# Kernel tuning notes

Hardware: AMD Instinct MI355X
Metric: run time of the kernel (lower is better)

## Reference

```python
import jax, jax.numpy as jnp
import numpy as np

N_HEADS = 8

def gcn_conv(x, edge_index, W, b):
    # PyG GCNConv: add self-loops, symmetric normalization, linear transform + bias
    N = x.shape[0]
    loop = jnp.arange(N)
    src = jnp.concatenate([edge_index[0], loop])
    dst = jnp.concatenate([edge_index[1], loop])
    deg = jax.ops.segment_sum(jnp.ones(src.shape[0], dtype=x.dtype), dst, num_segments=N)
    dinv = jax.lax.rsqrt(jnp.maximum(deg, 1.0))  # deg >= 1 due to self-loops
    norm = dinv[src] * dinv[dst]                 # [E+N]
    h = x @ W                                    # [N, out]
    msg = h[src] * norm[:, None]                 # gather + scale
    return jax.ops.segment_sum(msg, dst, num_segments=N) + b

def layer_norm(x, g, b):
    mu = jnp.mean(x, axis=-1, keepdims=True)
    var = jnp.mean((x - mu) ** 2, axis=-1, keepdims=True)
    return (x - mu) * jax.lax.rsqrt(var + 1e-5) * g + b

def mha(q, kv, Wq, Wk, Wv, Wo):
    B, M, d = q.shape
    dh = d // N_HEADS
    Q = (q @ Wq).reshape(B, M, N_HEADS, dh)
    K = (kv @ Wk).reshape(B, kv.shape[1], N_HEADS, dh)
    V = (kv @ Wv).reshape(B, kv.shape[1], N_HEADS, dh)
    scale = jnp.asarray(1.0 / np.sqrt(dh), q.dtype)
    scores = jnp.einsum('bqhd,bkhd->bhqk', Q, K) * scale
    attn = jax.nn.softmax(scores, axis=-1)
    out = jnp.einsum('bhqk,bkhd->bqhd', attn, V).reshape(B, M, d)
    return out @ Wo

def setup_inputs() -> dict:
    key = jax.random.key(0)
    ks = jax.random.split(key, 24)
    B, M, d, dff, L = 32, 1024, 128, 512, 2
    N, E = B * M, 524288
    s = 0.02
    inp = {
        'enc_out_vari': jax.random.normal(ks[0], (B, M, d), jnp.float32),
        'x_enc': jax.random.normal(ks[1], (B, M, d), jnp.float32),
        'x_raw': jax.random.normal(ks[2], (N, d), jnp.float32),
        'edge_index': jax.random.randint(ks[3], (2, E), 0, N, jnp.int64 if jax.config.jax_enable_x64 else jnp.int32),
        'W_gcn1': s * jax.random.normal(ks[4], (d, d), jnp.float32),
        'b_gcn1': jnp.zeros((d,), jnp.float32),
        'W_gcn2': s * jax.random.normal(ks[5], (d, d), jnp.float32),
        'b_gcn2': jnp.zeros((d,), jnp.float32),
        'Wq': s * jax.random.normal(ks[6], (L, d, d), jnp.float32),
        'Wk': s * jax.random.normal(ks[7], (L, d, d), jnp.float32),
        'Wv': s * jax.random.normal(ks[8], (L, d, d), jnp.float32),
        'Wo': s * jax.random.normal(ks[9], (L, d, d), jnp.float32),
        'Wff1': s * jax.random.normal(ks[10], (L, d, dff), jnp.float32),
        'bff1': jnp.zeros((L, dff), jnp.float32),
        'Wff2': s * jax.random.normal(ks[11], (L, dff, d), jnp.float32),
        'bff2': jnp.zeros((L, d), jnp.float32),
        'ln1_g': jnp.ones((L, d), jnp.float32),
        'ln1_b': jnp.zeros((L, d), jnp.float32),
        'ln2_g': jnp.ones((L, d), jnp.float32),
        'ln2_b': jnp.zeros((L, d), jnp.float32),
    }
    return inp

def reference(enc_out_vari, x_enc, x_raw, edge_index, W_gcn1, b_gcn1, W_gcn2, b_gcn2,
              Wq, Wk, Wv, Wo, Wff1, bff1, Wff2, bff2, ln1_g, ln1_b, ln2_g, ln2_b):
    B, M, d = enc_out_vari.shape
    # GCN stack (dropout is identity in eval mode)
    x1 = jax.nn.relu(gcn_conv(x_raw, edge_index, W_gcn1, b_gcn1))
    x2 = jax.nn.relu(gcn_conv(x1, edge_index, W_gcn2, b_gcn2))
    x = x2.reshape(B, M, d)
    # Transformer encoder: cross-attention from enc_out_vari onto GCN features
    y = enc_out_vari
    L = Wq.shape[0]
    for l in range(L):
        a = mha(y, x, Wq[l], Wk[l], Wv[l], Wo[l])
        y = layer_norm(y + a, ln1_g[l], ln1_b[l])
        f = jax.nn.relu(y @ Wff1[l] + bff1[l]) @ Wff2[l] + bff2[l]
        y = layer_norm(y + f, ln2_g[l], ln2_b[l])
    return y
```

## Files before the change

kernel.cpp:

```cpp
#include <hip/hip_runtime.h>
#include <math.h>


typedef __attribute__((ext_vector_type(8)))  short short8;
typedef __attribute__((ext_vector_type(4)))  float f32x4;
typedef __attribute__((ext_vector_type(16))) float f32x16;

__device__ __forceinline__ unsigned short f2bf(float x) {
    unsigned u = __builtin_bit_cast(unsigned, x);
    u = (u + 0x7FFFu + ((u >> 16) & 1u)) >> 16;
    return (unsigned short)u;
}
__device__ __forceinline__ float bflo(unsigned u) { return __builtin_bit_cast(float, u << 16); }
__device__ __forceinline__ float bfhi(unsigned u) { return __builtin_bit_cast(float, u & 0xffff0000u); }
__device__ __forceinline__ float fast_exp2(float x) {
    float r; asm("v_exp_f32 %0, %1" : "=v"(r) : "v"(x)); return r;
}

__global__ void count_kernel(const int* __restrict__ dst, int* __restrict__ cnt, int E) {
    int e = blockIdx.x * 256 + threadIdx.x;
    if (e < E) atomicAdd(&cnt[dst[e]], 1);
}

__global__ __launch_bounds__(256)
void scanA_kernel(const int* __restrict__ cnt, int* __restrict__ partial)
{
    __shared__ int wsum[4];
    int t = threadIdx.x;
    int v = cnt[blockIdx.x * 256 + t];
    #pragma unroll
    for (int off = 32; off; off >>= 1) v += __shfl_xor(v, off, 64);
    if ((t & 63) == 0) wsum[t >> 6] = v;
    __syncthreads();
    if (t == 0) partial[blockIdx.x] = wsum[0] + wsum[1] + wsum[2] + wsum[3];
}

__global__ __launch_bounds__(128)
void scanB_kernel(const int* __restrict__ partial, int* __restrict__ base)
{
    __shared__ int p[128];
    int t = threadIdx.x;
    int v = partial[t];
    p[t] = v;
    __syncthreads();
    for (int o = 1; o < 128; o <<= 1) {
        int q = (t >= o) ? p[t - o] : 0;
        __syncthreads();
        p[t] += q;
        __syncthreads();
    }
    base[t] = p[t] - v;
}

__global__ __launch_bounds__(256)
void scanC_kernel(const int* __restrict__ cnt, const int* __restrict__ base,
                  int* __restrict__ off, int* __restrict__ cursor,
                  float* __restrict__ dinv, int N, int E)
{
    __shared__ int p[256];
    int t = threadIdx.x, b = blockIdx.x;
    int i = b * 256 + t;
    int c = cnt[i];
    p[t] = c;
    __syncthreads();
    for (int o = 1; o < 256; o <<= 1) {
        int q = (t >= o) ? p[t - o] : 0;
        __syncthreads();
        p[t] += q;
        __syncthreads();
    }
    int ex = base[b] + p[t] - c;
    off[i] = ex;
    cursor[i] = ex;
    dinv[i] = rsqrtf((float)c + 1.0f);
    if (b == 0 && t == 0) off[N] = E;
}

__global__ void place_kernel(const int* __restrict__ src, const int* __restrict__ dst,
                             int* __restrict__ cursor, int* __restrict__ csr_src, int E)
{
    int e = blockIdx.x * 256 + threadIdx.x;
    if (e < E) {
        int p = atomicAdd(&cursor[dst[e]], 1);
        csr_src[p] = src[e];
    }
}

__global__ __launch_bounds__(256)
void prep_kernel(const float* __restrict__ xraw, unsigned short* __restrict__ xrawh,
                 const float* __restrict__ enc, float* __restrict__ bufY,
                 unsigned short* __restrict__ bufYh,
                 const float* Wg1, const float* Wg2, const float* Wq, const float* Wk,
                 const float* Wv, const float* Wo, const float* Wff1, const float* Wff2,
                 unsigned short* __restrict__ out, int nconv)
{
    const int bid = blockIdx.x, tid = threadIdx.x;
    if (bid < nconv) {
        int i = bid * 256 + tid;
        float4 v = ((const float4*)xraw)[i];
        ushort4 h; h.x = f2bf(v.x); h.y = f2bf(v.y); h.z = f2bf(v.z); h.w = f2bf(v.w);
        ((ushort4*)xrawh)[i] = h;
        return;
    }
    if (bid < 2 * nconv) {
        int i = (bid - nconv) * 256 + tid;
        float4 v = ((const float4*)enc)[i];
        ((float4*)bufY)[i] = v;
        ushort4 h; h.x = f2bf(v.x); h.y = f2bf(v.y); h.z = f2bf(v.z); h.w = f2bf(v.w);
        ((ushort4*)bufYh)[i] = h;
        return;
    }
    const int bid2 = bid - 2 * nconv;
    const int slot = bid2 >> 8;
    const int bx   = bid2 & 255;
    const float* src; int ks; int Ns; size_t doff; float scale = 1.0f;
    if      (slot == 0)  { src = Wg1;                        ks = 7; Ns = 128; doff = 0; }
    else if (slot == 1)  { src = Wg2;                        ks = 7; Ns = 128; doff = 16384; }
    else if (slot <= 3)  { src = Wq  + (slot - 2)  * 16384;  ks = 7; Ns = 128; doff = 32768  + (size_t)(slot - 2)  * 16384; scale = 0.36067376022f; }
    else if (slot <= 5)  { src = Wk  + (slot - 4)  * 16384;  ks = 7; Ns = 128; doff = 65536  + (size_t)(slot - 4)  * 32768; }
    else if (slot <= 7)  { src = Wv  + (slot - 6)  * 16384;  ks = 7; Ns = 128; doff = 65536  + (size_t)(slot - 6)  * 32768 + 16384; }
    else if (slot <= 9)  { src = Wo  + (slot - 8)  * 16384;  ks = 7; Ns = 128; doff = 131072 + (size_t)(slot - 8)  * 16384; }
    else if (slot <= 11) { src = Wff1 + (slot - 10) * 65536; ks = 7; Ns = 512; doff = 163840 + (size_t)(slot - 10) * 65536; }
    else                 { src = Wff2 + (slot - 12) * 65536; ks = 9; Ns = 128; doff = 294912 + (size_t)(slot - 12) * 65536; }
    const int total = Ns << ks;
    int id = bx * 256 + tid;
    if (id >= total) return;
    int n = id >> ks;
    int k = id & ((1 << ks) - 1);
    out[doff + id] = f2bf(src[(size_t)k * Ns + n] * scale);
}

__device__ __forceinline__
void gemm64_body(unsigned short* As, unsigned short* Ws,
                 const unsigned short* __restrict__ A,
                 const unsigned short* __restrict__ Wt,
                 void* __restrict__ C, void* __restrict__ C2, int K, int ldc,
                 const float* __restrict__ bias, const float* __restrict__ rowscale,
                 int relu, int mode, int bx, int by)
{
    const int tid  = threadIdx.x;
    const int lane = tid & 63, wave = tid >> 6;
    const int m31 = lane & 31, hi = lane >> 5;
    const int row0 = bx * 64;
    const int c0   = by * 64;
    const int wrow = (wave & 1) * 32;
    const int wcol = (wave >> 1) * 32;
    const int sr = tid >> 2, sk = (tid & 3) * 16;

    f32x16 acc = {};

    for (int kt = 0; kt < K; kt += 64) {
        if (kt) __syncthreads();
        *(short8*)&As[sr * 72 + sk]     = *(const short8*)&A [(size_t)(row0 + sr) * K + kt + sk];
        *(short8*)&As[sr * 72 + sk + 8] = *(const short8*)&A [(size_t)(row0 + sr) * K + kt + sk + 8];
        *(short8*)&Ws[sr * 72 + sk]     = *(const short8*)&Wt[(size_t)(c0   + sr) * K + kt + sk];
        *(short8*)&Ws[sr * 72 + sk + 8] = *(const short8*)&Wt[(size_t)(c0   + sr) * K + kt + sk + 8];
        __syncthreads();
        #pragma unroll
        for (int ks = 0; ks < 4; ++ks) {
            short8 af = *(const short8*)&As[(wrow + m31) * 72 + ks * 16 + hi * 8];
            short8 bf = *(const short8*)&Ws[(wcol + m31) * 72 + ks * 16 + hi * 8];
            acc = __builtin_amdgcn_mfma_f32_32x32x16_bf16(af, bf, acc, 0, 0, 0);
        }
    }

    const int col = c0 + wcol + m31;
    #pragma unroll
    for (int r = 0; r < 16; ++r) {
        const int row = row0 + wrow + (r & 3) + 8 * (r >> 2) + 4 * hi;
        float v = acc[r];
        if (rowscale) v *= rowscale[row];
        if (bias) v += bias[col];
        if (relu) v = fmaxf(v, 0.0f);
        if (mode == 1) {
            ((unsigned short*)C)[(size_t)row * ldc + col] = f2bf(v);
        } else {
            if (col < 128) {
                ((unsigned short*)C)[(size_t)row * 128 + col] = f2bf(v);
            } else {
                int ch = col - 128, hh = ch >> 4, dd = ch & 15;
                int kg = row & 1023;
                int w  = kg & 127;
                int kpos = (kg & ~127) | ((w & 15) * 8) | (w >> 4);
                ((unsigned short*)C2)[(((size_t)(row >> 10) * 8 + hh) * 16 + dd) * 1024
                                      + kpos] = f2bf(v);
            }
        }
    }
}

__global__ __launch_bounds__(256)
void gemm64_kernel(const unsigned short* __restrict__ A,
                   const unsigned short* __restrict__ Wt,
                   void* __restrict__ C, void* __restrict__ C2, int K,
                   const float* __restrict__ bias, const float* __restrict__ rowscale,
                   int relu, int mode)
{
    __shared__ unsigned short As[64 * 72];
    __shared__ unsigned short Ws[64 * 72];
    gemm64_body(As, Ws, A, Wt, C, C2, K, gridDim.y * 64, bias, rowscale, relu, mode,
                blockIdx.x, blockIdx.y);
}

__global__ __launch_bounds__(256)
void qkv_kernel(const unsigned short* __restrict__ Yh, const unsigned short* __restrict__ wtq,
                unsigned short* __restrict__ Qh,
                const unsigned short* __restrict__ Bh, const unsigned short* __restrict__ wtkv,
                unsigned short* __restrict__ Kg, unsigned short* __restrict__ Vtg)
{
    __shared__ unsigned short As[64 * 72];
    __shared__ unsigned short Ws[64 * 72];
    if (blockIdx.y < 2)
        gemm64_body(As, Ws, Yh, wtq, Qh, nullptr, 128, 128, nullptr, nullptr, 0, 1,
                    blockIdx.x, blockIdx.y);
    else
        gemm64_body(As, Ws, Bh, wtkv, Kg, Vtg, 128, 256, nullptr, nullptr, 0, 2,
                    blockIdx.x, blockIdx.y - 2);
}

__global__ __launch_bounds__(256)
void gemm_ln_kernel(const unsigned short* __restrict__ A,
                    const unsigned short* __restrict__ Wt, int K,
                    const float* __restrict__ bias,
                    const float* __restrict__ resid_in, float* __restrict__ resid_out,
                    unsigned short* __restrict__ yh,
                    const float* __restrict__ lng, const float* __restrict__ lnb)
{
    __shared__ __align__(16) unsigned char smraw[23040];
    unsigned short* As = (unsigned short*)smraw;
    unsigned short* Ws = (unsigned short*)(smraw + 4608);

    const int tid  = threadIdx.x;
    const int lane = tid & 63, wave = tid >> 6;
    const int m31 = lane & 31, hi = lane >> 5;
    const int row0 = blockIdx.x * 32;
    const int wcol = wave * 32;
    const int sr = tid >> 3, sk = (tid & 7) * 8;
    const int wr = tid >> 1, wo = (tid & 1) * 32;

    f32x16 acc = {};

    for (int kt = 0; kt < K; kt += 64) {
        if (kt) __syncthreads();
        *(short8*)&As[sr * 72 + sk]      = *(const short8*)&A [(size_t)(row0 + sr) * K + kt + sk];
        *(short8*)&Ws[wr * 72 + wo]      = *(const short8*)&Wt[(size_t)wr * K + kt + wo];
        *(short8*)&Ws[wr * 72 + wo + 8]  = *(const short8*)&Wt[(size_t)wr * K + kt + wo + 8];
        *(short8*)&Ws[wr * 72 + wo + 16] = *(const short8*)&Wt[(size_t)wr * K + kt + wo + 16];
        *(short8*)&Ws[wr * 72 + wo + 24] = *(const short8*)&Wt[(size_t)wr * K + kt + wo + 24];
        __syncthreads();
        #pragma unroll
        for (int ks = 0; ks < 4; ++ks) {
            short8 af = *(const short8*)&As[m31 * 72 + ks * 16 + hi * 8];
            short8 bf = *(const short8*)&Ws[(wcol + m31) * 72 + ks * 16 + hi * 8];
            acc = __builtin_amdgcn_mfma_f32_32x32x16_bf16(af, bf, acc, 0, 0, 0);
        }
    }

    __syncthreads();
    float* Ts = (float*)smraw;
    {
        const int col = wcol + m31;
        #pragma unroll
        for (int r = 0; r < 16; ++r) {
            const int rl = (r & 3) + 8 * (r >> 2) + 4 * hi;
            float v = acc[r];
            if (bias) v += bias[col];
            Ts[rl * 130 + col] = v;
        }
    }
    __syncthreads();
    const int r  = tid >> 3;
    const int cq = tid & 7;
    const int row = row0 + r;
    float v[16], s1 = 0.f, s2 = 0.f;
    const float* yr = resid_in + (size_t)row * 128 + cq * 16;
    #pragma unroll
    for (int i = 0; i < 4; ++i) {
        float4 yv = *(const float4*)&yr[i * 4];
        float ys[4] = {yv.x, yv.y, yv.z, yv.w};
        #pragma unroll
        for (int j = 0; j < 4; ++j) {
            float t = Ts[r * 130 + cq * 16 + i * 4 + j] + ys[j];
            v[i * 4 + j] = t; s1 += t; s2 += t * t;
        }
    }
    s1 += __shfl_xor(s1, 1, 64); s1 += __shfl_xor(s1, 2, 64); s1 += __shfl_xor(s1, 4, 64);
    s2 += __shfl_xor(s2, 1, 64); s2 += __shfl_xor(s2, 2, 64); s2 += __shfl_xor(s2, 4, 64);
    const float mu  = s1 * (1.0f / 128.0f);
    const float inv = rsqrtf(s2 * (1.0f / 128.0f) - mu * mu + 1e-5f);
    float* outr = resid_out + (size_t)row * 128 + cq * 16;
    unsigned short* yhr = yh + (size_t)row * 128 + cq * 16;
    #pragma unroll
    for (int i = 0; i < 4; ++i) {
        float o0 = (v[i*4+0] - mu) * inv * lng[cq*16 + i*4 + 0] + lnb[cq*16 + i*4 + 0];
        float o1 = (v[i*4+1] - mu) * inv * lng[cq*16 + i*4 + 1] + lnb[cq*16 + i*4 + 1];
        float o2 = (v[i*4+2] - mu) * inv * lng[cq*16 + i*4 + 2] + lnb[cq*16 + i*4 + 2];
        float o3 = (v[i*4+3] - mu) * inv * lng[cq*16 + i*4 + 3] + lnb[cq*16 + i*4 + 3];
        float4 ov; ov.x = o0; ov.y = o1; ov.z = o2; ov.w = o3;
        *(float4*)&outr[i * 4] = ov;
        ushort4 hv; hv.x = f2bf(o0); hv.y = f2bf(o1); hv.z = f2bf(o2); hv.w = f2bf(o3);
        *(ushort4*)&yhr[i * 4] = hv;
    }
}

__global__ __launch_bounds__(256)
void gather_kernel(const unsigned short* __restrict__ hs, const int* __restrict__ csr_off,
                   const int* __restrict__ csr_src, const float* __restrict__ dinv,
                   const float* __restrict__ bias, unsigned short* __restrict__ out, int N)
{
    const int node = blockIdx.x * 4 + (threadIdx.x >> 6);
    const int lane = threadIdx.x & 63;
    const int s0 = csr_off[node], s1 = csr_off[node + 1];
    const unsigned* hsu = (const unsigned*)hs;

    unsigned u = hsu[(size_t)node * 64 + lane];
    float a0 = bflo(u), a1 = bfhi(u);

    for (int base = s0; base < s1; base += 64) {
        int cnt = s1 - base; if (cnt > 64) cnt = 64;
        int idx = (base + lane < s1) ? csr_src[base + lane] : 0;
        int j = 0;
        for (; j + 4 <= cnt; j += 4) {
            size_t sA = (size_t)__shfl(idx, j,     64) * 64;
            size_t sB = (size_t)__shfl(idx, j + 1, 64) * 64;
            size_t sC = (size_t)__shfl(idx, j + 2, 64) * 64;
            size_t sD = (size_t)__shfl(idx, j + 3, 64) * 64;
            unsigned uA = hsu[sA + lane], uB = hsu[sB + lane];
            unsigned uC = hsu[sC + lane], uD = hsu[sD + lane];
            a0 += (bflo(uA) + bflo(uB)) + (bflo(uC) + bflo(uD));
            a1 += (bfhi(uA) + bfhi(uB)) + (bfhi(uC) + bfhi(uD));
        }
        for (; j < cnt; ++j) {
            size_t sb = (size_t)__shfl(idx, j, 64) * 64;
            unsigned ub = hsu[sb + lane];
            a0 += bflo(ub); a1 += bfhi(ub);
        }
    }
    float di = dinv[node];
    float v0 = fmaxf(a0 * di + bias[lane * 2],     0.0f);
    float v1 = fmaxf(a1 * di + bias[lane * 2 + 1], 0.0f);
    ((unsigned*)out)[(size_t)node * 64 + lane] =
        ((unsigned)f2bf(v1) << 16) | (unsigned)f2bf(v0);
}

__global__ __launch_bounds__(256)
void attn_mfma_kernel(const unsigned short* __restrict__ Qh,
                      const unsigned short* __restrict__ Kg,
                      const unsigned short* __restrict__ Vtg,
                      unsigned short* __restrict__ Obh)
{
    __shared__ __align__(16) unsigned short Ks[128 * 16];
    __shared__ __align__(16) unsigned short Vt[16 * 136];
    __shared__ __align__(16) unsigned short Ps[4][16 * 136];

    const int tid  = threadIdx.x;
    const int lane = tid & 63, wave = tid >> 6;
    const int quad = lane >> 4, l16 = lane & 15;
    const int q0 = blockIdx.x * 64, h = blockIdx.y, b = blockIdx.z;

    const int key  = tid >> 1, half = (tid & 1) * 8;
    const int dim  = tid >> 4, kc = (tid & 15) * 8;
    const unsigned short* Kp = &Kg[((size_t)b * 1024 + key) * 128 + h * 16 + half];
    const unsigned short* Vp = &Vtg[(((size_t)b * 8 + h) * 16 + dim) * 1024 + kc];

    short8 qa = {};
    if (quad < 2) {
        qa = *(const short8*)&Qh[((size_t)b * 1024 + q0 + wave * 16 + l16) * 128 + h * 16 + quad * 8];
    }

    f32x4 o = {0.f, 0.f, 0.f, 0.f};
    float l0[4] = {0.f, 0.f, 0.f, 0.f};
    unsigned short* Pw = &Ps[wave][0];
    const int kread = (quad & 1) * 8;

    short8 kreg = *(const short8*)(Kp);
    short8 vreg = *(const short8*)(Vp);

    for (int it = 0; it < 8; ++it) {
        *(short8*)&Ks[key * 16 + half] = kreg;
        *(short8*)&Vt[dim * 136 + kc]  = vreg;
        if (it < 7) {
            kreg = *(const short8*)(Kp + (size_t)(it + 1) * 128 * 128);
            vreg = *(const short8*)(Vp + (it + 1) * 128);
        }
        __syncthreads();

        f32x4 s[8];
        f32x4 zc = {0.f, 0.f, 0.f, 0.f};
        #pragma unroll
        for (int g = 0; g < 8; ++g) {
            short8 kb = *(const short8*)&Ks[(g * 16 + l16) * 16 + kread];
            s[g] = __builtin_amdgcn_mfma_f32_16x16x32_bf16(qa, kb, zc, 0, 0, 0);
        }

        #pragma unroll
        for (int r = 0; r < 4; ++r) {
            float p0 = fast_exp2(s[0][r]);
            float p1 = fast_exp2(s[1][r]);
            float p2 = fast_exp2(s[2][r]);
            float p3 = fast_exp2(s[3][r]);
            float p4 = fast_exp2(s[4][r]);
            float p5 = fast_exp2(s[5][r]);
            float p6 = fast_exp2(s[6][r]);
            float p7 = fast_exp2(s[7][r]);
            l0[r] += ((p0 + p1) + (p2 + p3)) + ((p4 + p5) + (p6 + p7));
            uint4 pk;
            pk.x = __builtin_amdgcn_perm(__builtin_bit_cast(unsigned, p1),
                                         __builtin_bit_cast(unsigned, p0), 0x07060302u);
            pk.y = __builtin_amdgcn_perm(__builtin_bit_cast(unsigned, p3),
                                         __builtin_bit_cast(unsigned, p2), 0x07060302u);
            pk.z = __builtin_amdgcn_perm(__builtin_bit_cast(unsigned, p5),
                                         __builtin_bit_cast(unsigned, p4), 0x07060302u);
            pk.w = __builtin_amdgcn_perm(__builtin_bit_cast(unsigned, p7),
                                         __builtin_bit_cast(unsigned, p6), 0x07060302u);
            *(uint4*)&Pw[(quad * 4 + r) * 136 + l16 * 8] = pk;
        }
        asm volatile("s_waitcnt lgkmcnt(0)" ::: "memory");
        __builtin_amdgcn_sched_barrier(0);

        #pragma unroll
        for (int t = 0; t < 4; ++t) {
            short8 pa = *(const short8*)&Pw[l16 * 136 + t * 32 + quad * 8];
            short8 vb = *(const short8*)&Vt[l16 * 136 + t * 32 + quad * 8];
            o = __builtin_amdgcn_mfma_f32_16x16x32_bf16(pa, vb, o, 0, 0, 0);
        }
        if (it < 7) __syncthreads();
    }

    #pragma unroll
    for (int r = 0; r < 4; ++r) {
        float lr = l0[r];
        #pragma unroll
        for (int off = 1; off < 16; off <<= 1) lr += __shfl_xor(lr, off, 64);
        float linv = 1.0f / lr;
        int qrow = q0 + wave * 16 + quad * 4 + r;
        Obh[((size_t)b * 1024 + qrow) * 128 + h * 16 + l16] = f2bf(o[r] * linv);
    }
}

extern "C" void kernel_launch(void* const* d_in, const int* in_sizes, int n_in,
                              void* d_out, int out_size, void* d_ws, size_t ws_size,
                              hipStream_t stream)
{
    const float* enc  = (const float*)d_in[0];
    const float* xraw = (const float*)d_in[2];
    const int*   ei   = (const int*)d_in[3];
    const float* Wg1  = (const float*)d_in[4];
    const float* bg1  = (const float*)d_in[5];
    const float* Wg2  = (const float*)d_in[6];
    const float* bg2  = (const float*)d_in[7];
    const float* Wq   = (const float*)d_in[8];
    const float* Wk   = (const float*)d_in[9];
    const float* Wv   = (const float*)d_in[10];
    const float* Wo   = (const float*)d_in[11];
    const float* Wff1 = (const float*)d_in[12];
    const float* bff1 = (const float*)d_in[13];
    const float* Wff2 = (const float*)d_in[14];
    const float* bff2 = (const float*)d_in[15];
    const float* ln1g = (const float*)d_in[16];
    const float* ln1b = (const float*)d_in[17];
    const float* ln2g = (const float*)d_in[18];
    const float* ln2b = (const float*)d_in[19];

    const int E  = in_sizes[3] / 2;
    const int N  = in_sizes[2] / 128;
    const int BM = in_sizes[0] / 128;
    const int B  = BM / 1024;
    const int L  = in_sizes[8] / (128 * 128);

    const int* srcE = ei;
    const int* dstE = ei + E;

    const size_t ND = (size_t)N * 128;

    float* ws   = (float*)d_ws;
    float* dinv = ws;
    int* cnt     = (int*)(ws + 32768);
    int* csr_off = cnt + N;
    int* cursor  = csr_off + N + 4;
    int* csr_src = cursor + N;
    int* partial = csr_src + E;
    int* pbase   = partial + 128;
    float* bufY  = (float*)(((uintptr_t)(pbase + 128) + 255) & ~(uintptr_t)255);
    unsigned short* ush   = (unsigned short*)(bufY + ND);
    unsigned short* bufYh = ush;
    unsigned short* bufBh = bufYh + ND;
    unsigned short* region = bufBh + ND;
    unsigned short* Qh  = region;
    unsigned short* Kg  = region + ND;
    unsigned short* Vtg = region + 2 * ND;
    unsigned short* Th  = region + 3 * ND;
    unsigned short* Hh  = region;
    unsigned short* hsh   = region;
    unsigned short* xrawh = region + ND;
    unsigned short* wt  = region + 4 * ND;

    hipMemsetAsync(cnt, 0, (size_t)N * sizeof(int), stream);
    count_kernel<<<(E + 255) / 256, 256, 0, stream>>>(dstE, cnt, E);
    scanA_kernel<<<N / 256, 256, 0, stream>>>(cnt, partial);
    scanB_kernel<<<1, 128, 0, stream>>>(partial, pbase);
    scanC_kernel<<<N / 256, 256, 0, stream>>>(cnt, pbase, csr_off, cursor, dinv, N, E);
    place_kernel<<<(E + 255) / 256, 256, 0, stream>>>(srcE, dstE, cursor, csr_src, E);

    const int nconv = (int)(ND / 1024);
    prep_kernel<<<2 * nconv + 14 * 256, 256, 0, stream>>>(
        xraw, xrawh, enc, bufY, bufYh,
        Wg1, Wg2, Wq, Wk, Wv, Wo, Wff1, Wff2, wt, nconv);

    gemm64_kernel<<<dim3(N / 64, 2), 256, 0, stream>>>(xrawh, wt, hsh, nullptr, 128,
        nullptr, dinv, 0, 1);
    gather_kernel<<<N / 4, 256, 0, stream>>>(hsh, csr_off, csr_src, dinv, bg1, bufBh, N);
    gemm64_kernel<<<dim3(N / 64, 2), 256, 0, stream>>>(bufBh, wt + 16384, hsh, nullptr, 128,
        nullptr, dinv, 0, 1);
    gather_kernel<<<N / 4, 256, 0, stream>>>(hsh, csr_off, csr_src, dinv, bg2, bufBh, N);

    for (int l = 0; l < L; ++l) {
        const unsigned short* wtq  = wt + 32768  + (size_t)l * 16384;
        const unsigned short* wtkv = wt + 65536  + (size_t)l * 32768;
        const unsigned short* wto  = wt + 131072 + (size_t)l * 16384;
        const unsigned short* wtf1 = wt + 163840 + (size_t)l * 65536;
        const unsigned short* wtf2 = wt + 294912 + (size_t)l * 65536;

        qkv_kernel<<<dim3(BM / 64, 6), 256, 0, stream>>>(bufYh, wtq, Qh,
                                                         bufBh, wtkv, Kg, Vtg);

        attn_mfma_kernel<<<dim3(16, 8, B), 256, 0, stream>>>(Qh, Kg, Vtg, Th);

        gemm_ln_kernel<<<BM / 32, 256, 0, stream>>>(Th, wto, 128, nullptr,
            bufY, bufY, bufYh, ln1g + l * 128, ln1b + l * 128);

        gemm64_kernel<<<dim3(BM / 64, 8), 256, 0, stream>>>(bufYh, wtf1, Hh, nullptr, 128,
            bff1 + l * 512, nullptr, 1, 1);

        float* rout = (l == L - 1) ? (float*)d_out : bufY;
        gemm_ln_kernel<<<BM / 32, 256, 0, stream>>>(Hh, wtf2, 512, bff2 + l * 128,
            bufY, rout, bufYh, ln2g + l * 128, ln2b + l * 128);
    }
}
```

Baseline: 523.1 us.

## Keep attention probabilities in registers via transposed QK MFMA and permuted V layout

The QK^T MFMA now runs with operands swapped, so each lane holds score values already laid out as the A-operand of the PV MFMA. The probabilities are packed to bf16 in registers instead of going through a per-wave LDS buffer. The V-transpose write in the GEMM epilogue is re-permuted so key order matches this register layout. The row-sum is computed with an extra MFMA against a ones vector, which replaces the scalar adds and shuffle reduction. This removes the LDS round trip, the waitcnt and the sched barrier, at the cost of doubling MFMA work in the PV stage and summing probabilities after bf16 rounding.

```diff
diff --git a/kernel.cpp b/kernel.cpp
--- a/kernel.cpp
+++ b/kernel.cpp
@@ -181,7 +181,9 @@
                 int ch = col - 128, hh = ch >> 4, dd = ch & 15;
                 int kg = row & 1023;
                 int w  = kg & 127;
-                int kpos = (kg & ~127) | ((w & 15) * 8) | (w >> 4);
+                int slot = ((w >> 5) << 5) | (((w >> 2) & 3) << 3)
+                         | (((w >> 4) & 1) << 2) | (w & 3);
+                int kpos = (kg & ~127) | slot;
                 ((unsigned short*)C2)[(((size_t)(row >> 10) * 8 + hh) * 16 + dd) * 1024
                                       + kpos] = f2bf(v);
             }
@@ -351,7 +353,6 @@
 {
     __shared__ __align__(16) unsigned short Ks[128 * 16];
     __shared__ __align__(16) unsigned short Vt[16 * 136];
-    __shared__ __align__(16) unsigned short Ps[4][16 * 136];
 
     const int tid  = threadIdx.x;
     const int lane = tid & 63, wave = tid >> 6;
@@ -368,9 +369,12 @@
         qa = *(const short8*)&Qh[((size_t)b * 1024 + q0 + wave * 16 + l16) * 128 + h * 16 + quad * 8];
     }
 
-    f32x4 o = {0.f, 0.f, 0.f, 0.f};
-    float l0[4] = {0.f, 0.f, 0.f, 0.f};
-    unsigned short* Pw = &Ps[wave][0];
+    const short one_bf = (short)0x3F80;
+    const short8 onesv = {one_bf, one_bf, one_bf, one_bf,
+                          one_bf, one_bf, one_bf, one_bf};
+
+    f32x4 o    = {0.f, 0.f, 0.f, 0.f};
+    f32x4 lacc = {0.f, 0.f, 0.f, 0.f};
     const int kread = (quad & 1) * 8;
 
     short8 kreg = *(const short8*)(Kp);
@@ -390,49 +394,39 @@
         #pragma unroll
         for (int g = 0; g < 8; ++g) {
             short8 kb = *(const short8*)&Ks[(g * 16 + l16) * 16 + kread];
-            s[g] = __builtin_amdgcn_mfma_f32_16x16x32_bf16(qa, kb, zc, 0, 0, 0);
-        }
-
-        #pragma unroll
-        for (int r = 0; r < 4; ++r) {
-            float p0 = fast_exp2(s[0][r]);
-            float p1 = fast_exp2(s[1][r]);
-            float p2 = fast_exp2(s[2][r]);
-            float p3 = fast_exp2(s[3][r]);
-            float p4 = fast_exp2(s[4][r]);
-            float p5 = fast_exp2(s[5][r]);
-            float p6 = fast_exp2(s[6][r]);
-            float p7 = fast_exp2(s[7][r]);
-            l0[r] += ((p0 + p1) + (p2 + p3)) + ((p4 + p5) + (p6 + p7));
-            uint4 pk;
-            pk.x = __builtin_amdgcn_perm(__builtin_bit_cast(unsigned, p1),
-                                         __builtin_bit_cast(unsigned, p0), 0x07060302u);
-            pk.y = __builtin_amdgcn_perm(__builtin_bit_cast(unsigned, p3),
-                                         __builtin_bit_cast(unsigned, p2), 0x07060302u);
-            pk.z = __builtin_amdgcn_perm(__builtin_bit_cast(unsigned, p5),
-                                         __builtin_bit_cast(unsigned, p4), 0x07060302u);
-            pk.w = __builtin_amdgcn_perm(__builtin_bit_cast(unsigned, p7),
-                                         __builtin_bit_cast(unsigned, p6), 0x07060302u);
-            *(uint4*)&Pw[(quad * 4 + r) * 136 + l16 * 8] = pk;
-        }
-        asm volatile("s_waitcnt lgkmcnt(0)" ::: "memory");
-        __builtin_amdgcn_sched_barrier(0);
+            s[g] = __builtin_amdgcn_mfma_f32_16x16x32_bf16(kb, qa, zc, 0, 0, 0);
+        }
 
         #pragma unroll
         for (int t = 0; t < 4; ++t) {
-            short8 pa = *(const short8*)&Pw[l16 * 136 + t * 32 + quad * 8];
+            float p00 = fast_exp2(s[2*t][0]);
+            float p01 = fast_exp2(s[2*t][1]);
+            float p02 = fast_exp2(s[2*t][2]);
+            float p03 = fast_exp2(s[2*t][3]);
+            float p10 = fast_exp2(s[2*t+1][0]);
+            float p11 = fast_exp2(s[2*t+1][1]);
+            float p12 = fast_exp2(s[2*t+1][2]);
+            float p13 = fast_exp2(s[2*t+1][3]);
+            uint4 pk;
+            pk.x = __builtin_amdgcn_perm(__builtin_bit_cast(unsigned, p01),
+                                         __builtin_bit_cast(unsigned, p00), 0x07060302u);
+            pk.y = __builtin_amdgcn_perm(__builtin_bit_cast(unsigned, p03),
+                                         __builtin_bit_cast(unsigned, p02), 0x07060302u);
+            pk.z = __builtin_amdgcn_perm(__builtin_bit_cast(unsigned, p11),
+                                         __builtin_bit_cast(unsigned, p10), 0x07060302u);
+            pk.w = __builtin_amdgcn_perm(__builtin_bit_cast(unsigned, p13),
+                                         __builtin_bit_cast(unsigned, p12), 0x07060302u);
+            short8 pa = __builtin_bit_cast(short8, pk);
             short8 vb = *(const short8*)&Vt[l16 * 136 + t * 32 + quad * 8];
-            o = __builtin_amdgcn_mfma_f32_16x16x32_bf16(pa, vb, o, 0, 0, 0);
+            o    = __builtin_amdgcn_mfma_f32_16x16x32_bf16(pa, vb, o, 0, 0, 0);
+            lacc = __builtin_amdgcn_mfma_f32_16x16x32_bf16(pa, onesv, lacc, 0, 0, 0);
         }
         if (it < 7) __syncthreads();
     }
 
     #pragma unroll
     for (int r = 0; r < 4; ++r) {
-        float lr = l0[r];
-        #pragma unroll
-        for (int off = 1; off < 16; off <<= 1) lr += __shfl_xor(lr, off, 64);
-        float linv = 1.0f / lr;
+        float linv = 1.0f / lacc[r];
         int qrow = q0 + wave * 16 + quad * 4 + r;
         Obh[((size_t)b * 1024 + qrow) * 128 + h * 16 + l16] = f2bf(o[r] * linv);
     }
```

Result: faster. 482.3 us (-7.8%).
